# Optimization experiments

Measured on AMD Instinct MI355X. Metric: run time of the kernel, lower is better.

## Reference

```python
import jax, jax.numpy as jnp
import numpy as np

B = 65536
D_IN = 8
H1, H2 = 256, 256


def setup_inputs() -> dict:
    key = jax.random.key(0)
    ks = jax.random.split(key, 12)
    def lin(kw, kb, fan_in, fan_out):
        s = 1.0 / np.sqrt(fan_in)
        W = jax.random.uniform(kw, (fan_out, fan_in), jnp.float32, -s, s)
        b = jax.random.uniform(kb, (fan_out,), jnp.float32, -s, s)
        return W, b
    W0, b0 = lin(ks[0], ks[1], D_IN, H1)
    W1, b1 = lin(ks[2], ks[3], H1, H2)
    W2, b2 = lin(ks[4], ks[5], H2, 1)
    W3, b3 = lin(ks[6], ks[7], 1, 8)
    x_batch = jax.random.normal(ks[8], (B, D_IN), jnp.float32)
    scores_x_batch = jax.random.normal(ks[9], (B, D_IN), jnp.float32)
    c = jnp.zeros((), jnp.float32)  # init_val parameter
    return {"x_batch": x_batch, "scores_x_batch": scores_x_batch,
            "W0": W0, "b0": b0, "W1": W1, "b1": b1,
            "W2": W2, "b2": b2, "W3": W3, "b3": b3, "c": c}


def reference(x_batch, scores_x_batch, W0, b0, W1, b1, W2, b2, W3, b3, c):
    # singleforwardpass: tanh on all layers except the last
    def single(x):  # x: [8] -> [8]
        y = jnp.tanh(W0 @ x + b0)
        y = jnp.tanh(W1 @ y + b1)
        y = jnp.tanh(W2 @ y + b2)
        return W3 @ y + b3

    eye = jnp.eye(D_IN, dtype=x_batch.dtype)

    def per_sample(x, score):
        # jacobian(single, x).diag().sum() + dot(single(x), score) + c
        u, lin_fn = jax.linearize(single, x)
        J = jax.vmap(lin_fn)(eye)        # [8, 8] (columns of Jacobian as rows)
        div = jnp.trace(J)               # sum of Jacobian diagonal
        return c + div + jnp.dot(u, score)

    return jax.vmap(per_sample)(x_batch, scores_x_batch)  # [B]
```

## Files before the change

kernel.cpp:

```cpp
#include <hip/hip_runtime.h>
#include <hip/hip_bf16.h>

#define B_TOTAL 65536
#define H 256
#define TS 32
#define THREADS 256
#define STRIDE 264

typedef __attribute__((ext_vector_type(8))) short bf16x8;
typedef __attribute__((ext_vector_type(4))) float f32x4;

__device__ __forceinline__ void tanh_r(float x, float& t, float& r) {
    float e = __expf(x + x);
    r = __builtin_amdgcn_rcpf(e + 1.0f);
    t = fmaf(-2.0f, r, 1.0f);
}
__device__ __forceinline__ float bf2f(ushort b) {
    union { unsigned u; float f; } v; v.u = ((unsigned)b) << 16;
    return v.f;
}
__device__ __forceinline__ ushort f2bf(float f) {
    union { float f; unsigned u; } v; v.f = f;
    unsigned r = v.u + 0x7fffu + ((v.u >> 16) & 1u);
    return (ushort)(r >> 16);
}
__device__ __forceinline__ ushort2 cvt2(float a, float b) {
    union { __hip_bfloat162 h; ushort2 u; } v;
    v.h = __float22bfloat162_rn(make_float2(a, b));
    return v.u;
}
__device__ __forceinline__ bf16x8 pack8(float4 a, float4 b) {
    union { bf16x8 v; ushort2 u[4]; } r;
    r.u[0] = cvt2(a.x, a.y); r.u[1] = cvt2(a.z, a.w);
    r.u[2] = cvt2(b.x, b.y); r.u[3] = cvt2(b.z, b.w);
    return r.v;
}

__global__ void pack_weights(const float* __restrict__ W1, ushort* __restrict__ pack) {
    int g = blockIdx.x * 256 + threadIdx.x;
    int jt = g >> 9;
    int ks = (g >> 6) & 7;
    int l  = g & 63;
    int row = jt * 16 + (l & 15);
    int k0  = ks * 32 + (l >> 4) * 8;
    ushort* dst = pack + (size_t)g * 8;
    const float* src = W1 + (size_t)row * H + k0;
#pragma unroll
    for (int t = 0; t < 8; ++t) dst[t] = f2bf(src[t]);
}

__launch_bounds__(THREADS, 4)
__global__ void fused_mlp(const float* __restrict__ x_batch,
                          const float* __restrict__ scores,
                          const float* __restrict__ W0, const float* __restrict__ b0,
                          const float* __restrict__ b1,
                          const float* __restrict__ W2, const float* __restrict__ b2,
                          const float* __restrict__ W3, const float* __restrict__ b3,
                          const float* __restrict__ cptr,
                          const ushort* __restrict__ packs,
                          float* __restrict__ out) {
    __shared__ ushort Y0[TS][STRIDE];
    __shared__ ushort DG[TS][STRIDE];
    __shared__ float  G0[H];
    __shared__ float  Z2p[4][TS];
    __shared__ float  Trp[4][TS];

    const int tid  = threadIdx.x;
    const int lane = tid & 63;
    const int w    = tid >> 6;
    const int bs   = blockIdx.x * TS;
    const int cl   = lane & 15;
    const int q    = lane >> 4;
    const int rq   = q * 4;
    const int j0   = w * 64;

    const ushort* pW = packs + (size_t)(4 * w) * 4096 + (size_t)lane * 8;

    {
        const float* wr = W0 + (size_t)tid * 8;
        float4 wa = *(const float4*)wr, wb = *(const float4*)(wr + 4);
        float4 w3a = *(const float4*)W3, w3b = *(const float4*)(W3 + 4);
        G0[tid] = wa.x * w3a.x + wa.y * w3a.y + wa.z * w3a.z + wa.w * w3a.w
                + wb.x * w3b.x + wb.y * w3b.y + wb.z * w3b.z + wb.w * w3b.w;
    }

    f32x4 l0[4][2];
    {
        bf16x8 bx[2];
#pragma unroll
        for (int st = 0; st < 2; ++st) {
            bf16x8 p = (bf16x8){0, 0, 0, 0, 0, 0, 0, 0};
            if (q == 0) {
                const float* xr = x_batch + (size_t)(bs + st * 16 + cl) * 8;
                p = pack8(*(const float4*)xr, *(const float4*)(xr + 4));
            }
            bx[st] = p;
        }
#pragma unroll
        for (int jt = 0; jt < 4; ++jt) {
            const float* wr = W0 + (size_t)(j0 + jt * 16 + cl) * 8;
            bf16x8 af = pack8(*(const float4*)wr, *(const float4*)(wr + 4));
#pragma unroll
            for (int st = 0; st < 2; ++st) {
                f32x4 z = (f32x4){0.f, 0.f, 0.f, 0.f};
                l0[jt][st] = __builtin_amdgcn_mfma_f32_16x16x32_bf16(af, bx[st], z, 0, 0, 0);
            }
        }
    }
    __syncthreads();

    {
#pragma unroll
        for (int jt = 0; jt < 4; ++jt) {
            float4 bv = *(const float4*)(b0 + j0 + jt * 16 + rq);
            float4 gv = *(const float4*)&G0[j0 + jt * 16 + rq];
#pragma unroll
            for (int st = 0; st < 2; ++st) {
                const int row = st * 16 + cl;
                f32x4 z = l0[jt][st];
                float t0, t1, t2, t3, r0, r1, r2, r3;
                tanh_r(z[0] + bv.x, t0, r0); tanh_r(z[1] + bv.y, t1, r1);
                tanh_r(z[2] + bv.z, t2, r2); tanh_r(z[3] + bv.w, t3, r3);
                ushort2 lo = cvt2(t0, t1), hi = cvt2(t2, t3);
                ushort4 vv; vv.x = lo.x; vv.y = lo.y; vv.z = hi.x; vv.w = hi.y;
                *(ushort4*)&Y0[row][j0 + jt * 16 + rq] = vv;
                float m0 = 4.f * r0, m1 = 4.f * r1, m2 = 4.f * r2, m3 = 4.f * r3;
                float d0 = fmaf(-m0, r0, m0), d1 = fmaf(-m1, r1, m1);
                float d2 = fmaf(-m2, r2, m2), d3 = fmaf(-m3, r3, m3);
                lo = cvt2(d0 * gv.x, d1 * gv.y); hi = cvt2(d2 * gv.z, d3 * gv.w);
                vv.x = lo.x; vv.y = lo.y; vv.z = hi.x; vv.w = hi.y;
                *(ushort4*)&DG[row][j0 + jt * 16 + rq] = vv;
            }
        }
    }

    bf16x8 wf0_ = *(const bf16x8*)(pW);
    bf16x8 wf1_ = *(const bf16x8*)(pW + 4096);
    bf16x8 wf2_ = *(const bf16x8*)(pW + 8192);
    bf16x8 wf3_ = *(const bf16x8*)(pW + 12288);

    __syncthreads();

    f32x4 facc[4][2], bacc[4][2];
#pragma unroll
    for (int jj = 0; jj < 4; ++jj)
#pragma unroll
        for (int stl = 0; stl < 2; ++stl) {
            facc[jj][stl] = (f32x4){0.f, 0.f, 0.f, 0.f};
            bacc[jj][stl] = (f32x4){0.f, 0.f, 0.f, 0.f};
        }
#pragma unroll 1
    for (int ks = 0; ks < 8; ++ks) {
        bf16x8 wn0 = wf0_, wn1 = wf1_, wn2 = wf2_, wn3 = wf3_;
        if (ks < 7) {
            const ushort* pn = pW + (size_t)(ks + 1) * 512;
            wn0 = *(const bf16x8*)(pn);
            wn1 = *(const bf16x8*)(pn + 4096);
            wn2 = *(const bf16x8*)(pn + 8192);
            wn3 = *(const bf16x8*)(pn + 12288);
        }
        const int k0 = ks * 32 + q * 8;
#pragma unroll
        for (int stl = 0; stl < 2; ++stl) {
            bf16x8 by = *(const bf16x8*)&Y0[stl * 16 + cl][k0];
            bf16x8 bd = *(const bf16x8*)&DG[stl * 16 + cl][k0];
            facc[0][stl] = __builtin_amdgcn_mfma_f32_16x16x32_bf16(wf0_, by, facc[0][stl], 0, 0, 0);
            bacc[0][stl] = __builtin_amdgcn_mfma_f32_16x16x32_bf16(wf0_, bd, bacc[0][stl], 0, 0, 0);
            facc[1][stl] = __builtin_amdgcn_mfma_f32_16x16x32_bf16(wf1_, by, facc[1][stl], 0, 0, 0);
            bacc[1][stl] = __builtin_amdgcn_mfma_f32_16x16x32_bf16(wf1_, bd, bacc[1][stl], 0, 0, 0);
            facc[2][stl] = __builtin_amdgcn_mfma_f32_16x16x32_bf16(wf2_, by, facc[2][stl], 0, 0, 0);
            bacc[2][stl] = __builtin_amdgcn_mfma_f32_16x16x32_bf16(wf2_, bd, bacc[2][stl], 0, 0, 0);
            facc[3][stl] = __builtin_amdgcn_mfma_f32_16x16x32_bf16(wf3_, by, facc[3][stl], 0, 0, 0);
            bacc[3][stl] = __builtin_amdgcn_mfma_f32_16x16x32_bf16(wf3_, bd, bacc[3][stl], 0, 0, 0);
        }
        wf0_ = wn0; wf1_ = wn1; wf2_ = wn2; wf3_ = wn3;
    }

    {
        float4 b1v[4], w2v[4];
#pragma unroll
        for (int jj = 0; jj < 4; ++jj) {
            b1v[jj] = *(const float4*)(b1 + j0 + jj * 16 + rq);
            w2v[jj] = *(const float4*)(W2 + j0 + jj * 16 + rq);
        }
#pragma unroll
        for (int stl = 0; stl < 2; ++stl) {
            float zp = 0.f, tp = 0.f;
#pragma unroll
            for (int jj = 0; jj < 4; ++jj) {
                f32x4 z  = facc[jj][stl];
                f32x4 mm = bacc[jj][stl];
                float4 bv = b1v[jj];
                float4 wv = w2v[jj];
                float t0, t1, t2, t3, r0, r1, r2, r3;
                tanh_r(z[0] + bv.x, t0, r0); tanh_r(z[1] + bv.y, t1, r1);
                tanh_r(z[2] + bv.z, t2, r2); tanh_r(z[3] + bv.w, t3, r3);
                zp = fmaf(wv.x, t0, zp); zp = fmaf(wv.y, t1, zp);
                zp = fmaf(wv.z, t2, zp); zp = fmaf(wv.w, t3, zp);
                float m0 = 4.f * wv.x * r0, m1 = 4.f * wv.y * r1;
                float m2 = 4.f * wv.z * r2, m3 = 4.f * wv.w * r3;
                float a0 = fmaf(-m0, r0, m0), a1 = fmaf(-m1, r1, m1);
                float a2 = fmaf(-m2, r2, m2), a3 = fmaf(-m3, r3, m3);
                tp = fmaf(a0, mm[0], tp); tp = fmaf(a1, mm[1], tp);
                tp = fmaf(a2, mm[2], tp); tp = fmaf(a3, mm[3], tp);
            }
            zp += __shfl_xor(zp, 16);
            zp += __shfl_xor(zp, 32);
            tp += __shfl_xor(tp, 16);
            tp += __shfl_xor(tp, 32);
            if (lane < 16) {
                Z2p[w][stl * 16 + lane] = zp;
                Trp[w][stl * 16 + lane] = tp;
            }
        }
    }
    __syncthreads();

    if (tid < TS) {
        const int s = tid;
        float z2 = b2[0], tr = 0.f;
#pragma unroll
        for (int k = 0; k < 4; ++k) { z2 += Z2p[k][s]; tr += Trp[k][s]; }
        float y2, r2;
        tanh_r(z2, y2, r2);
        float m2 = 4.0f * r2;
        float dy2 = fmaf(-m2, r2, m2);
        float4 w3a = *(const float4*)W3;
        float4 w3b = *(const float4*)(W3 + 4);
        float4 b3a = *(const float4*)b3;
        float4 b3b = *(const float4*)(b3 + 4);
        const float* sc = scores + (size_t)(bs + s) * 8;
        float4 s0 = *(const float4*)sc;
        float4 s1 = *(const float4*)(sc + 4);
        float p1 = w3a.x * s0.x + w3a.y * s0.y + w3a.z * s0.z + w3a.w * s0.w
                 + w3b.x * s1.x + w3b.y * s1.y + w3b.z * s1.z + w3b.w * s1.w;
        float p2 = b3a.x * s0.x + b3a.y * s0.y + b3a.z * s0.z + b3a.w * s0.w
                 + b3b.x * s1.x + b3b.y * s1.y + b3b.z * s1.z + b3b.w * s1.w;
        out[bs + s] = cptr[0] + dy2 * tr + fmaf(y2, p1, p2);
    }
}

extern "C" void kernel_launch(void* const* d_in, const int* in_sizes, int n_in,
                              void* d_out, int out_size, void* d_ws, size_t ws_size,
                              hipStream_t stream) {
    const float* x  = (const float*)d_in[0];
    const float* sc = (const float*)d_in[1];
    const float* W0 = (const float*)d_in[2];
    const float* b0 = (const float*)d_in[3];
    const float* W1 = (const float*)d_in[4];
    const float* b1 = (const float*)d_in[5];
    const float* W2 = (const float*)d_in[6];
    const float* b2 = (const float*)d_in[7];
    const float* W3 = (const float*)d_in[8];
    const float* b3 = (const float*)d_in[9];
    const float* c  = (const float*)d_in[10];
    float* out = (float*)d_out;
    ushort* packs = (ushort*)d_ws;

    hipLaunchKernelGGL(pack_weights, dim3(32), dim3(256), 0, stream, W1, packs);
    hipLaunchKernelGGL(fused_mlp, dim3(B_TOTAL / TS), dim3(THREADS), 0, stream,
                       x, sc, W0, b0, b1, W2, b2, W3, b3, c, packs, out);
}
```

Measured before the change: 35.17 us.

## Process four sample tiles per block with double-buffered layer-0 staging

Each block now handles four 32-sample tiles instead of one, keeping the W0 fragments in registers and computing the next tile's first-layer MFMA and tanh epilogue into a second LDS buffer while the current tile runs its layer-1 MFMAs. This spreads per-block setup (G0, W0 packing) across more samples and aims to overlap the first-layer work with the second layer. W1 fragments are now reloaded from global/L2 for every tile with a fully unrolled loop instead of register prefetching. Occupancy drops (launch bounds 2, doubled LDS) and the grid shrinks to 512 blocks, which risks underfilling the GPU.

```diff
diff --git a/kernel.cpp b/kernel.cpp
--- a/kernel.cpp
+++ b/kernel.cpp
@@ -4,6 +4,7 @@
 #define B_TOTAL 65536
 #define H 256
 #define TS 32
+#define NT 4
 #define THREADS 256
 #define STRIDE 264
 
@@ -49,7 +50,7 @@
     for (int t = 0; t < 8; ++t) dst[t] = f2bf(src[t]);
 }
 
-__launch_bounds__(THREADS, 4)
+__launch_bounds__(THREADS, 2)
 __global__ void fused_mlp(const float* __restrict__ x_batch,
                           const float* __restrict__ scores,
                           const float* __restrict__ W0, const float* __restrict__ b0,
@@ -59,16 +60,16 @@
                           const float* __restrict__ cptr,
                           const ushort* __restrict__ packs,
                           float* __restrict__ out) {
-    __shared__ ushort Y0[TS][STRIDE];
-    __shared__ ushort DG[TS][STRIDE];
+    __shared__ ushort Y0[2][TS][STRIDE];
+    __shared__ ushort DG[2][TS][STRIDE];
     __shared__ float  G0[H];
-    __shared__ float  Z2p[4][TS];
-    __shared__ float  Trp[4][TS];
+    __shared__ float  Z2p[4][NT][TS];
+    __shared__ float  Trp[4][NT][TS];
 
     const int tid  = threadIdx.x;
     const int lane = tid & 63;
     const int w    = tid >> 6;
-    const int bs   = blockIdx.x * TS;
+    const int bs0  = blockIdx.x * (TS * NT);
     const int cl   = lane & 15;
     const int q    = lane >> 4;
     const int rq   = q * 4;
@@ -84,143 +85,141 @@
                 + wb.x * w3b.x + wb.y * w3b.y + wb.z * w3b.z + wb.w * w3b.w;
     }
 
+    bf16x8 af[4];
+#pragma unroll
+    for (int jt = 0; jt < 4; ++jt) {
+        const float* wr = W0 + (size_t)(j0 + jt * 16 + cl) * 8;
+        af[jt] = pack8(*(const float4*)wr, *(const float4*)(wr + 4));
+    }
+
     f32x4 l0[4][2];
-    {
-        bf16x8 bx[2];
-#pragma unroll
-        for (int st = 0; st < 2; ++st) {
-            bf16x8 p = (bf16x8){0, 0, 0, 0, 0, 0, 0, 0};
-            if (q == 0) {
-                const float* xr = x_batch + (size_t)(bs + st * 16 + cl) * 8;
-                p = pack8(*(const float4*)xr, *(const float4*)(xr + 4));
+
+#define A_MFMA(tt)                                                              \
+    {                                                                           \
+        bf16x8 bx0 = (bf16x8){0,0,0,0,0,0,0,0}, bx1 = bx0;                      \
+        if (q == 0) {                                                           \
+            const float* xr0 = x_batch + (size_t)(bs0 + (tt) * TS + cl) * 8;    \
+            const float* xr1 = xr0 + 128;                                       \
+            bx0 = pack8(*(const float4*)xr0, *(const float4*)(xr0 + 4));        \
+            bx1 = pack8(*(const float4*)xr1, *(const float4*)(xr1 + 4));        \
+        }                                                                       \
+        _Pragma("unroll")                                                       \
+        for (int jt = 0; jt < 4; ++jt) {                                        \
+            f32x4 zz = (f32x4){0.f, 0.f, 0.f, 0.f};                             \
+            l0[jt][0] = __builtin_amdgcn_mfma_f32_16x16x32_bf16(af[jt], bx0, zz, 0, 0, 0); \
+            l0[jt][1] = __builtin_amdgcn_mfma_f32_16x16x32_bf16(af[jt], bx1, zz, 0, 0, 0); \
+        }                                                                       \
+    }
+
+#define A_EPI(bb)                                                               \
+    {                                                                           \
+        _Pragma("unroll")                                                       \
+        for (int jt = 0; jt < 4; ++jt) {                                        \
+            float4 bv = *(const float4*)(b0 + j0 + jt * 16 + rq);               \
+            float4 gv = *(const float4*)&G0[j0 + jt * 16 + rq];                 \
+            _Pragma("unroll")                                                   \
+            for (int st = 0; st < 2; ++st) {                                    \
+                const int row = st * 16 + cl;                                   \
+                f32x4 z = l0[jt][st];                                           \
+                float t0, t1, t2, t3, r0, r1, r2, r3;                           \
+                tanh_r(z[0] + bv.x, t0, r0); tanh_r(z[1] + bv.y, t1, r1);       \
+                tanh_r(z[2] + bv.z, t2, r2); tanh_r(z[3] + bv.w, t3, r3);       \
+                ushort2 lo = cvt2(t0, t1), hi = cvt2(t2, t3);                   \
+                ushort4 vv; vv.x = lo.x; vv.y = lo.y; vv.z = hi.x; vv.w = hi.y; \
+                *(ushort4*)&Y0[bb][row][j0 + jt * 16 + rq] = vv;                \
+                float m0 = 4.f * r0, m1 = 4.f * r1, m2 = 4.f * r2, m3 = 4.f * r3; \
+                float d0 = fmaf(-m0, r0, m0), d1 = fmaf(-m1, r1, m1);           \
+                float d2 = fmaf(-m2, r2, m2), d3 = fmaf(-m3, r3, m3);           \
+                lo = cvt2(d0 * gv.x, d1 * gv.y); hi = cvt2(d2 * gv.z, d3 * gv.w); \
+                vv.x = lo.x; vv.y = lo.y; vv.z = hi.x; vv.w = hi.y;             \
+                *(ushort4*)&DG[bb][row][j0 + jt * 16 + rq] = vv;                \
+            }                                                                   \
+        }                                                                       \
+    }
+
+    A_MFMA(0)
+    __syncthreads();
+    A_EPI(0)
+    __syncthreads();
+
+#pragma unroll
+    for (int t = 0; t < NT; ++t) {
+        const int rb = t & 1;
+        if (t + 1 < NT) A_MFMA(t + 1)
+
+        f32x4 facc[4][2], bacc[4][2];
+#pragma unroll
+        for (int jj = 0; jj < 4; ++jj)
+#pragma unroll
+            for (int stl = 0; stl < 2; ++stl) {
+                facc[jj][stl] = (f32x4){0.f, 0.f, 0.f, 0.f};
+                bacc[jj][stl] = (f32x4){0.f, 0.f, 0.f, 0.f};
             }
-            bx[st] = p;
-        }
-#pragma unroll
-        for (int jt = 0; jt < 4; ++jt) {
-            const float* wr = W0 + (size_t)(j0 + jt * 16 + cl) * 8;
-            bf16x8 af = pack8(*(const float4*)wr, *(const float4*)(wr + 4));
-#pragma unroll
-            for (int st = 0; st < 2; ++st) {
-                f32x4 z = (f32x4){0.f, 0.f, 0.f, 0.f};
-                l0[jt][st] = __builtin_amdgcn_mfma_f32_16x16x32_bf16(af, bx[st], z, 0, 0, 0);
+#pragma unroll
+        for (int ks = 0; ks < 8; ++ks) {
+            const ushort* pk = pW + (size_t)ks * 512;
+            bf16x8 wf0 = *(const bf16x8*)(pk);
+            bf16x8 wf1 = *(const bf16x8*)(pk + 4096);
+            bf16x8 wf2 = *(const bf16x8*)(pk + 8192);
+            bf16x8 wf3 = *(const bf16x8*)(pk + 12288);
+            const int k0 = ks * 32 + q * 8;
+#pragma unroll
+            for (int stl = 0; stl < 2; ++stl) {
+                bf16x8 by = *(const bf16x8*)&Y0[rb][stl * 16 + cl][k0];
+                bf16x8 bd = *(const bf16x8*)&DG[rb][stl * 16 + cl][k0];
+                facc[0][stl] = __builtin_amdgcn_mfma_f32_16x16x32_bf16(wf0, by, facc[0][stl], 0, 0, 0);
+                bacc[0][stl] = __builtin_amdgcn_mfma_f32_16x16x32_bf16(wf0, bd, bacc[0][stl], 0, 0, 0);
+                facc[1][stl] = __builtin_amdgcn_mfma_f32_16x16x32_bf16(wf1, by, facc[1][stl], 0, 0, 0);
+                bacc[1][stl] = __builtin_amdgcn_mfma_f32_16x16x32_bf16(wf1, bd, bacc[1][stl], 0, 0, 0);
+                facc[2][stl] = __builtin_amdgcn_mfma_f32_16x16x32_bf16(wf2, by, facc[2][stl], 0, 0, 0);
+                bacc[2][stl] = __builtin_amdgcn_mfma_f32_16x16x32_bf16(wf2, bd, bacc[2][stl], 0, 0, 0);
+                facc[3][stl] = __builtin_amdgcn_mfma_f32_16x16x32_bf16(wf3, by, facc[3][stl], 0, 0, 0);
+                bacc[3][stl] = __builtin_amdgcn_mfma_f32_16x16x32_bf16(wf3, bd, bacc[3][stl], 0, 0, 0);
             }
         }
-    }
-    __syncthreads();
-
-    {
-#pragma unroll
-        for (int jt = 0; jt < 4; ++jt) {
-            float4 bv = *(const float4*)(b0 + j0 + jt * 16 + rq);
-            float4 gv = *(const float4*)&G0[j0 + jt * 16 + rq];
-#pragma unroll
-            for (int st = 0; st < 2; ++st) {
-                const int row = st * 16 + cl;
-                f32x4 z = l0[jt][st];
-                float t0, t1, t2, t3, r0, r1, r2, r3;
-                tanh_r(z[0] + bv.x, t0, r0); tanh_r(z[1] + bv.y, t1, r1);
-                tanh_r(z[2] + bv.z, t2, r2); tanh_r(z[3] + bv.w, t3, r3);
-                ushort2 lo = cvt2(t0, t1), hi = cvt2(t2, t3);
-                ushort4 vv; vv.x = lo.x; vv.y = lo.y; vv.z = hi.x; vv.w = hi.y;
-                *(ushort4*)&Y0[row][j0 + jt * 16 + rq] = vv;
-                float m0 = 4.f * r0, m1 = 4.f * r1, m2 = 4.f * r2, m3 = 4.f * r3;
-                float d0 = fmaf(-m0, r0, m0), d1 = fmaf(-m1, r1, m1);
-                float d2 = fmaf(-m2, r2, m2), d3 = fmaf(-m3, r3, m3);
-                lo = cvt2(d0 * gv.x, d1 * gv.y); hi = cvt2(d2 * gv.z, d3 * gv.w);
-                vv.x = lo.x; vv.y = lo.y; vv.z = hi.x; vv.w = hi.y;
-                *(ushort4*)&DG[row][j0 + jt * 16 + rq] = vv;
+
+        if (t + 1 < NT) A_EPI((t + 1) & 1)
+
+        {
+#pragma unroll
+            for (int stl = 0; stl < 2; ++stl) {
+                float zp = 0.f, tp = 0.f;
+#pragma unroll
+                for (int jj = 0; jj < 4; ++jj) {
+                    float4 bv = *(const float4*)(b1 + j0 + jj * 16 + rq);
+                    float4 wv = *(const float4*)(W2 + j0 + jj * 16 + rq);
+                    f32x4 z  = facc[jj][stl];
+                    f32x4 mm = bacc[jj][stl];
+                    float t0, t1, t2, t3, r0, r1, r2, r3;
+                    tanh_r(z[0] + bv.x, t0, r0); tanh_r(z[1] + bv.y, t1, r1);
+                    tanh_r(z[2] + bv.z, t2, r2); tanh_r(z[3] + bv.w, t3, r3);
+                    zp = fmaf(wv.x, t0, zp); zp = fmaf(wv.y, t1, zp);
+                    zp = fmaf(wv.z, t2, zp); zp = fmaf(wv.w, t3, zp);
+                    float m0 = 4.f * wv.x * r0, m1 = 4.f * wv.y * r1;
+                    float m2 = 4.f * wv.z * r2, m3 = 4.f * wv.w * r3;
+                    float a0 = fmaf(-m0, r0, m0), a1 = fmaf(-m1, r1, m1);
+                    float a2 = fmaf(-m2, r2, m2), a3 = fmaf(-m3, r3, m3);
+                    tp = fmaf(a0, mm[0], tp); tp = fmaf(a1, mm[1], tp);
+                    tp = fmaf(a2, mm[2], tp); tp = fmaf(a3, mm[3], tp);
+                }
+                zp += __shfl_xor(zp, 16);
+                zp += __shfl_xor(zp, 32);
+                tp += __shfl_xor(tp, 16);
+                tp += __shfl_xor(tp, 32);
+                if (lane < 16) {
+                    Z2p[w][t][stl * 16 + lane] = zp;
+                    Trp[w][t][stl * 16 + lane] = tp;
+                }
             }
         }
-    }
-
-    bf16x8 wf0_ = *(const bf16x8*)(pW);
-    bf16x8 wf1_ = *(const bf16x8*)(pW + 4096);
-    bf16x8 wf2_ = *(const bf16x8*)(pW + 8192);
-    bf16x8 wf3_ = *(const bf16x8*)(pW + 12288);
-
-    __syncthreads();
-
-    f32x4 facc[4][2], bacc[4][2];
-#pragma unroll
-    for (int jj = 0; jj < 4; ++jj)
-#pragma unroll
-        for (int stl = 0; stl < 2; ++stl) {
-            facc[jj][stl] = (f32x4){0.f, 0.f, 0.f, 0.f};
-            bacc[jj][stl] = (f32x4){0.f, 0.f, 0.f, 0.f};
-        }
-#pragma unroll 1
-    for (int ks = 0; ks < 8; ++ks) {
-        bf16x8 wn0 = wf0_, wn1 = wf1_, wn2 = wf2_, wn3 = wf3_;
-        if (ks < 7) {
-            const ushort* pn = pW + (size_t)(ks + 1) * 512;
-            wn0 = *(const bf16x8*)(pn);
-            wn1 = *(const bf16x8*)(pn + 4096);
-            wn2 = *(const bf16x8*)(pn + 8192);
-            wn3 = *(const bf16x8*)(pn + 12288);
-        }
-        const int k0 = ks * 32 + q * 8;
-#pragma unroll
-        for (int stl = 0; stl < 2; ++stl) {
-            bf16x8 by = *(const bf16x8*)&Y0[stl * 16 + cl][k0];
-            bf16x8 bd = *(const bf16x8*)&DG[stl * 16 + cl][k0];
-            facc[0][stl] = __builtin_amdgcn_mfma_f32_16x16x32_bf16(wf0_, by, facc[0][stl], 0, 0, 0);
-            bacc[0][stl] = __builtin_amdgcn_mfma_f32_16x16x32_bf16(wf0_, bd, bacc[0][stl], 0, 0, 0);
-            facc[1][stl] = __builtin_amdgcn_mfma_f32_16x16x32_bf16(wf1_, by, facc[1][stl], 0, 0, 0);
-            bacc[1][stl] = __builtin_amdgcn_mfma_f32_16x16x32_bf16(wf1_, bd, bacc[1][stl], 0, 0, 0);
-            facc[2][stl] = __builtin_amdgcn_mfma_f32_16x16x32_bf16(wf2_, by, facc[2][stl], 0, 0, 0);
-            bacc[2][stl] = __builtin_amdgcn_mfma_f32_16x16x32_bf16(wf2_, bd, bacc[2][stl], 0, 0, 0);
-            facc[3][stl] = __builtin_amdgcn_mfma_f32_16x16x32_bf16(wf3_, by, facc[3][stl], 0, 0, 0);
-            bacc[3][stl] = __builtin_amdgcn_mfma_f32_16x16x32_bf16(wf3_, bd, bacc[3][stl], 0, 0, 0);
-        }
-        wf0_ = wn0; wf1_ = wn1; wf2_ = wn2; wf3_ = wn3;
-    }
-
-    {
-        float4 b1v[4], w2v[4];
-#pragma unroll
-        for (int jj = 0; jj < 4; ++jj) {
-            b1v[jj] = *(const float4*)(b1 + j0 + jj * 16 + rq);
-            w2v[jj] = *(const float4*)(W2 + j0 + jj * 16 + rq);
-        }
-#pragma unroll
-        for (int stl = 0; stl < 2; ++stl) {
-            float zp = 0.f, tp = 0.f;
-#pragma unroll
-            for (int jj = 0; jj < 4; ++jj) {
-                f32x4 z  = facc[jj][stl];
-                f32x4 mm = bacc[jj][stl];
-                float4 bv = b1v[jj];
-                float4 wv = w2v[jj];
-                float t0, t1, t2, t3, r0, r1, r2, r3;
-                tanh_r(z[0] + bv.x, t0, r0); tanh_r(z[1] + bv.y, t1, r1);
-                tanh_r(z[2] + bv.z, t2, r2); tanh_r(z[3] + bv.w, t3, r3);
-                zp = fmaf(wv.x, t0, zp); zp = fmaf(wv.y, t1, zp);
-                zp = fmaf(wv.z, t2, zp); zp = fmaf(wv.w, t3, zp);
-                float m0 = 4.f * wv.x * r0, m1 = 4.f * wv.y * r1;
-                float m2 = 4.f * wv.z * r2, m3 = 4.f * wv.w * r3;
-                float a0 = fmaf(-m0, r0, m0), a1 = fmaf(-m1, r1, m1);
-                float a2 = fmaf(-m2, r2, m2), a3 = fmaf(-m3, r3, m3);
-                tp = fmaf(a0, mm[0], tp); tp = fmaf(a1, mm[1], tp);
-                tp = fmaf(a2, mm[2], tp); tp = fmaf(a3, mm[3], tp);
-            }
-            zp += __shfl_xor(zp, 16);
-            zp += __shfl_xor(zp, 32);
-            tp += __shfl_xor(tp, 16);
-            tp += __shfl_xor(tp, 32);
-            if (lane < 16) {
-                Z2p[w][stl * 16 + lane] = zp;
-                Trp[w][stl * 16 + lane] = tp;
-            }
-        }
-    }
-    __syncthreads();
-
-    if (tid < TS) {
-        const int s = tid;
+        __syncthreads();
+    }
+
+    if (tid < TS * NT) {
+        const int t = tid >> 5, i = tid & 31;
         float z2 = b2[0], tr = 0.f;
 #pragma unroll
-        for (int k = 0; k < 4; ++k) { z2 += Z2p[k][s]; tr += Trp[k][s]; }
+        for (int k = 0; k < 4; ++k) { z2 += Z2p[k][t][i]; tr += Trp[k][t][i]; }
         float y2, r2;
         tanh_r(z2, y2, r2);
         float m2 = 4.0f * r2;
@@ -229,15 +228,17 @@
         float4 w3b = *(const float4*)(W3 + 4);
         float4 b3a = *(const float4*)b3;
         float4 b3b = *(const float4*)(b3 + 4);
-        const float* sc = scores + (size_t)(bs + s) * 8;
+        const float* sc = scores + (size_t)(bs0 + tid) * 8;
         float4 s0 = *(const float4*)sc;
         float4 s1 = *(const float4*)(sc + 4);
         float p1 = w3a.x * s0.x + w3a.y * s0.y + w3a.z * s0.z + w3a.w * s0.w
                  + w3b.x * s1.x + w3b.y * s1.y + w3b.z * s1.z + w3b.w * s1.w;
         float p2 = b3a.x * s0.x + b3a.y * s0.y + b3a.z * s0.z + b3a.w * s0.w
                  + b3b.x * s1.x + b3b.y * s1.y + b3b.z * s1.z + b3b.w * s1.w;
-        out[bs + s] = cptr[0] + dy2 * tr + fmaf(y2, p1, p2);
-    }
+        out[bs0 + tid] = cptr[0] + dy2 * tr + fmaf(y2, p1, p2);
+    }
+#undef A_MFMA
+#undef A_EPI
 }
 
 extern "C" void kernel_launch(void* const* d_in, const int* in_sizes, int n_in,
@@ -258,6 +259,6 @@
     ushort* packs = (ushort*)d_ws;
 
     hipLaunchKernelGGL(pack_weights, dim3(32), dim3(256), 0, stream, W1, packs);
-    hipLaunchKernelGGL(fused_mlp, dim3(B_TOTAL / TS), dim3(THREADS), 0, stream,
+    hipLaunchKernelGGL(fused_mlp, dim3(B_TOTAL / (TS * NT)), dim3(THREADS), 0, stream,
                        x, sc, W0, b0, b1, W2, b2, W3, b3, c, packs, out);
 }
```

Result: slower. 36.46 us (+3.7%).
